# Kernel tuning notes

Hardware: AMD Instinct MI355X
Metric: run time of the kernel (lower is better)

Reference implementation:

```python
import jax, jax.numpy as jnp
import numpy as np

NEG = -1e30


def _layernorm(x, g, b, eps=1e-6):
    mu = jnp.mean(x, axis=-1, keepdims=True)
    var = jnp.mean((x - mu) ** 2, axis=-1, keepdims=True)
    return (x - mu) * jax.lax.rsqrt(var + eps) * g + b


def _ctc_loss(log_probs, targets, input_lengths, target_lengths, blank):
    # log_probs: (T, B, V); targets: (B, L) int; lengths: (B,) int
    T, B, V = log_probs.shape
    L = targets.shape[1]
    S = 2 * L + 1
    # extended target sequence: blank, t0, blank, t1, ..., blank
    ext = jnp.full((B, S), blank, dtype=targets.dtype)
    ext = ext.at[:, 1::2].set(targets)
    # skip transition allowed where label differs from label two back and is not blank
    ext_m2 = jnp.pad(ext, ((0, 0), (2, 0)), constant_values=blank)[:, :S]
    skip_mask = (jnp.arange(S)[None, :] >= 2) & (ext != ext_m2) & (ext != blank)
    # gather per-step emission log-probs for extended labels: (T, B, S)
    lp_ext = jnp.take_along_axis(
        log_probs, jnp.broadcast_to(ext[None], (T, B, S)), axis=2
    )

    alpha0 = jnp.full((B, S), NEG, dtype=log_probs.dtype)
    alpha0 = alpha0.at[:, 0].set(lp_ext[0, :, 0])
    alpha0 = alpha0.at[:, 1].set(lp_ext[0, :, 1])

    def step(alpha, lp_e):
        a1 = jnp.pad(alpha, ((0, 0), (1, 0)), constant_values=NEG)[:, :S]
        a2 = jnp.pad(alpha, ((0, 0), (2, 0)), constant_values=NEG)[:, :S]
        a2 = jnp.where(skip_mask, a2, NEG)
        new = jnp.logaddexp(jnp.logaddexp(alpha, a1), a2) + lp_e
        return new, new

    _, alphas_rest = jax.lax.scan(step, alpha0, lp_ext[1:])
    alphas = jnp.concatenate([alpha0[None], alphas_rest], axis=0)  # (T, B, S)

    alpha_T = alphas[input_lengths - 1, jnp.arange(B)]  # (B, S)
    s_end = 2 * target_lengths  # final blank position
    l_blank = jnp.take_along_axis(alpha_T, s_end[:, None], axis=1)[:, 0]
    l_label = jnp.take_along_axis(alpha_T, (s_end - 1)[:, None], axis=1)[:, 0]
    loss_b = -jnp.logaddexp(l_blank, l_label)
    # zero_infinity=True
    loss_b = jnp.where(loss_b > 1e29, 0.0, loss_b)
    # reduction='mean': divide each loss by its target length, then batch-mean
    return jnp.mean(loss_b / target_lengths.astype(loss_b.dtype))


def setup_inputs() -> dict:
    T, B, D, V, L = 2000, 32, 768, 1024, 150
    key = jax.random.key(0)
    ks = jax.random.split(key, 8)
    s = 0.02
    return {
        "source_encoder_output": jax.random.normal(ks[0], (T, B, D), jnp.float32),
        "W_proj": jax.random.normal(ks[1], (D, D), jnp.float32) * s,
        "b_proj": jnp.zeros((D,), jnp.float32),
        "W_tr": jax.random.normal(ks[2], (D, D), jnp.float32) * s,
        "b_tr": jnp.zeros((D,), jnp.float32),
        "ln_g": jnp.ones((D,), jnp.float32),
        "ln_b": jnp.zeros((D,), jnp.float32),
        "W_dec": jax.random.normal(ks[3], (D, V), jnp.float32) * s,
        "b_dec": jnp.zeros((V,), jnp.float32),
        "target_syllabe_ids": jax.random.randint(ks[4], (B, L), 1, V, jnp.int32),
        "source_encoder_output_lengths": jnp.full((B,), T, jnp.int32),
        "target_syllabe_id_lengths": jnp.full((B,), L, jnp.int32),
    }


def reference(source_encoder_output, W_proj, b_proj, W_tr, b_tr, ln_g, ln_b,
              W_dec, b_dec, target_syllabe_ids, source_encoder_output_lengths,
              target_syllabe_id_lengths):
    BLANK = 0
    x = source_encoder_output @ W_proj + b_proj          # encoder_projection
    x = jax.nn.gelu(x @ W_tr + b_tr, approximate=False)  # transform dense + gelu
    x = _layernorm(x, ln_g, ln_b, eps=1e-6)
    scores = x @ W_dec + b_dec                           # acoustic_decoder
    log_probs = jax.nn.log_softmax(scores, axis=-1)      # (T, B, V)
    return _ctc_loss(log_probs, target_syllabe_ids,
                     source_encoder_output_lengths,
                     target_syllabe_id_lengths, BLANK)
```

## Files before the change

### kernel.cpp

```cpp
#include <hip/hip_runtime.h>
#include <hip/hip_bf16.h>
#include <math.h>
#include <stdint.h>

#define NEGF (-1e30f)
#define LOG2E 1.44269504088896340736f
#define LN2 0.69314718055994530942f

#define LPROW 512

typedef short bf16x8 __attribute__((ext_vector_type(8)));
typedef float f32x4 __attribute__((ext_vector_type(4)));

__device__ __forceinline__ unsigned short f2b(float x) {
  __hip_bfloat16 h = __float2bfloat16(x);
  return *reinterpret_cast<unsigned short*>(&h);
}
__device__ __forceinline__ float b2f(unsigned short u) {
  __hip_bfloat16 h;
  *reinterpret_cast<unsigned short*>(&h) = u;
  return __bfloat162float(h);
}
__device__ __forceinline__ float gelu_exact(float x) {
  return 0.5f * x * (1.0f + erff(x * 0.70710678118654752440f));
}

#if __has_builtin(__builtin_amdgcn_logf)
__device__ __forceinline__ float fast_log2(float x) { return __builtin_amdgcn_logf(x); }
#else
__device__ __forceinline__ float fast_log2(float x) { return log2f(x); }
#endif

template<int CTRL>
__device__ __forceinline__ float dpp_shr(float x) {
  return __int_as_float(__builtin_amdgcn_update_dpp(
      0, __float_as_int(x), 0x110 | CTRL, 0xf, 0xf, true));
}
__device__ __forceinline__ float readlane_f(float x, int l) {
  return __int_as_float(__builtin_amdgcn_readlane(__float_as_int(x), l));
}

__device__ __forceinline__ uint4 gload_x4(const void* p) {
  uint4 r;
  asm volatile("global_load_dwordx4 %0, %1, off" : "=v"(r) : "v"(p));
  return r;
}

__device__ __forceinline__ void gload16(void* lds, const void* g) {
  __builtin_amdgcn_global_load_lds(
      (__attribute__((address_space(1))) void*)(uintptr_t)g,
      (__attribute__((address_space(3))) void*)(unsigned int)(uintptr_t)lds,
      16, 0, 0);
}

__global__ __launch_bounds__(256) void cvt_enc_kernel(
    const float* __restrict__ in, unsigned short* __restrict__ out, long n4)
{
  long i = (long)blockIdx.x * blockDim.x + threadIdx.x;
  const long stride = (long)gridDim.x * blockDim.x;
  for (; i < n4; i += stride) {
    float4 v = ((const float4*)in)[i];
    ushort4 o;
    o.x = f2b(v.x); o.y = f2b(v.y); o.z = f2b(v.z); o.w = f2b(v.w);
    ((ushort4*)out)[i] = o;
  }
}

__global__ __launch_bounds__(256) void cvt_wt_kernel(
    const float* __restrict__ W, unsigned short* __restrict__ WT, int K, int N)
{
  __shared__ float tile[32][33];
  const int n0 = blockIdx.x * 32, k0 = blockIdx.y * 32;
  const int tx = threadIdx.x, ty = threadIdx.y;
#pragma unroll
  for (int i = 0; i < 32; i += 8) {
    int k = k0 + ty + i, n = n0 + tx;
    tile[ty + i][tx] = (k < K && n < N) ? W[(long)k * N + n] : 0.f;
  }
  __syncthreads();
#pragma unroll
  for (int i = 0; i < 32; i += 8) {
    int n = n0 + ty + i, k = k0 + tx;
    if (n < N && k < K) WT[(long)n * K + k] = f2b(tile[tx][ty + i]);
  }
}

template<int NFULL, int EPI>
__global__ __launch_bounds__(256, 2) void gemm128_kernel(
    const unsigned short* __restrict__ A,
    const unsigned short* __restrict__ WT,
    const float* __restrict__ bias,
    unsigned short* __restrict__ out,
    float2* __restrict__ partials,
    int K)
{
  extern __shared__ char smem[];
  unsigned short* As = (unsigned short*)smem;
  unsigned short* Bs = (unsigned short*)(smem + 16384);

  const int tid = threadIdx.x, lane = tid & 63, w = tid >> 6;
  const int wr = w >> 1, wc = w & 1;
  const int cl = lane & 15, g = lane >> 4;
  const int bx = blockIdx.x;
  const long row0 = (long)blockIdx.y * 128;
  const int col0 = bx * 128;

  const int ch0 = w * 64 + lane;
  const int ch1 = 256 + ch0;
  const unsigned short* Ag0 = A + (row0 + (ch0 >> 2)) * K + (ch0 & 3) * 8;
  const unsigned short* Ag1 = A + (row0 + (ch1 >> 2)) * K + (ch1 & 3) * 8;
  const unsigned short* Bg0 = WT + (long)(col0 + (ch0 >> 2)) * K + (ch0 & 3) * 8;
  const unsigned short* Bg1 = WT + (long)(col0 + (ch1 >> 2)) * K + (ch1 & 3) * 8;
  unsigned short* Al0 = As + w * 512;
  unsigned short* Al1 = As + 2048 + w * 512;
  unsigned short* Bl0 = Bs + w * 512;
  unsigned short* Bl1 = Bs + 2048 + w * 512;

#define STAGE(buf, kt)                          \
  do {                                          \
    const int _ko = (kt) * 32;                  \
    gload16(Al0 + (buf) * 4096, Ag0 + _ko);     \
    gload16(Al1 + (buf) * 4096, Ag1 + _ko);     \
    gload16(Bl0 + (buf) * 4096, Bg0 + _ko);     \
    gload16(Bl1 + (buf) * 4096, Bg1 + _ko);     \
  } while (0)

  f32x4 acc[4][4];
#pragma unroll
  for (int mt = 0; mt < 4; ++mt)
#pragma unroll
    for (int nt = 0; nt < 4; ++nt) acc[mt][nt] = (f32x4){0.f, 0.f, 0.f, 0.f};

  const int NKT = K / 32;
  STAGE(0, 0);
  __syncthreads();
  int buf = 0;
  for (int kt = 0; kt < NKT; ++kt) {
    if (kt + 1 < NKT) STAGE(buf ^ 1, kt + 1);
    const unsigned short* Ab = As + buf * 4096;
    const unsigned short* Bb = Bs + buf * 4096;
    bf16x8 af[4], bfr[4];
#pragma unroll
    for (int mt = 0; mt < 4; ++mt)
      af[mt] = *(const bf16x8*)&Ab[(((wr * 64 + mt * 16 + cl) << 2) + g) * 8];
#pragma unroll
    for (int nt = 0; nt < 4; ++nt)
      bfr[nt] = *(const bf16x8*)&Bb[(((wc * 64 + nt * 16 + cl) << 2) + g) * 8];
#pragma unroll
    for (int mt = 0; mt < 4; ++mt)
#pragma unroll
      for (int nt = 0; nt < 4; ++nt)
        acc[mt][nt] = __builtin_amdgcn_mfma_f32_16x16x32_bf16(
            af[mt], bfr[nt], acc[mt][nt], 0, 0, 0);
    __syncthreads();
    buf ^= 1;
  }
#undef STAGE

  float bv[4];
#pragma unroll
  for (int nt = 0; nt < 4; ++nt) bv[nt] = bias[col0 + wc * 64 + nt * 16 + cl];
#pragma unroll
  for (int mt = 0; mt < 4; ++mt)
#pragma unroll
    for (int nt = 0; nt < 4; ++nt)
#pragma unroll
      for (int j = 0; j < 4; ++j) {
        float v = acc[mt][nt][j] + bv[nt];
        if (EPI == 1) v = gelu_exact(v);
        acc[mt][nt][j] = v;
      }

  if (EPI == 2) {
#pragma unroll
    for (int mt = 0; mt < 4; ++mt)
#pragma unroll
      for (int j = 0; j < 4; ++j) {
        float mx = fmaxf(fmaxf(acc[mt][0][j], acc[mt][1][j]),
                         fmaxf(acc[mt][2][j], acc[mt][3][j]));
#pragma unroll
        for (int off = 1; off < 16; off <<= 1)
          mx = fmaxf(mx, __shfl_xor(mx, off));
        float sm = 0.f;
#pragma unroll
        for (int nt = 0; nt < 4; ++nt) sm += expf(acc[mt][nt][j] - mx);
#pragma unroll
        for (int off = 1; off < 16; off <<= 1) sm += __shfl_xor(sm, off);
        if (cl == 0) {
          long m = row0 + wr * 64 + mt * 16 + g * 4 + j;
          partials[m * 16 + bx * 2 + wc] = make_float2(mx, sm);
        }
      }
  }

  unsigned short* Ct = (unsigned short*)smem;
#pragma unroll
  for (int mt = 0; mt < 4; ++mt)
#pragma unroll
    for (int nt = 0; nt < 4; ++nt)
#pragma unroll
      for (int j = 0; j < 4; ++j)
        Ct[(wr * 64 + mt * 16 + g * 4 + j) * 136 + wc * 64 + nt * 16 + cl] =
            f2b(acc[mt][nt][j]);
  __syncthreads();
  for (int idx = tid; idx < 2048; idx += 256) {
    int r = idx >> 4, ch = idx & 15;
    *(bf16x8*)&out[(row0 + r) * NFULL + col0 + ch * 8] =
        *(const bf16x8*)&Ct[r * 136 + ch * 8];
  }
}

template<int D>
__global__ __launch_bounds__(256) void ln_bf16_kernel(
    unsigned short* __restrict__ X, const float* __restrict__ g,
    const float* __restrict__ bt, long M)
{
  constexpr int NI = D / 256;
  const int lane = threadIdx.x & 63;
  const int wid = threadIdx.x >> 6;
  const long row = (long)blockIdx.x * 4 + wid;
  if (row >= M) return;

  float v[NI * 4];
  float s = 0.f;
#pragma unroll
  for (int i = 0; i < NI; ++i) {
    ushort4 u = *(const ushort4*)&X[row * D + (i * 64 + lane) * 4];
    v[i * 4 + 0] = b2f(u.x); v[i * 4 + 1] = b2f(u.y);
    v[i * 4 + 2] = b2f(u.z); v[i * 4 + 3] = b2f(u.w);
    s += v[i * 4 + 0] + v[i * 4 + 1] + v[i * 4 + 2] + v[i * 4 + 3];
  }
#pragma unroll
  for (int off = 32; off; off >>= 1) s += __shfl_xor(s, off);
  const float mu = s * (1.0f / D);
  float q = 0.f;
#pragma unroll
  for (int i = 0; i < NI * 4; ++i) { float d = v[i] - mu; q += d * d; }
#pragma unroll
  for (int off = 32; off; off >>= 1) q += __shfl_xor(q, off);
  const float rs = rsqrtf(q * (1.0f / D) + 1e-6f);
#pragma unroll
  for (int i = 0; i < NI; ++i) {
    ushort4 o;
    int c = (i * 64 + lane) * 4;
    o.x = f2b((v[i * 4 + 0] - mu) * rs * g[c + 0] + bt[c + 0]);
    o.y = f2b((v[i * 4 + 1] - mu) * rs * g[c + 1] + bt[c + 1]);
    o.z = f2b((v[i * 4 + 2] - mu) * rs * g[c + 2] + bt[c + 2]);
    o.w = f2b((v[i * 4 + 3] - mu) * rs * g[c + 3] + bt[c + 3]);
    *(ushort4*)&X[row * D + c] = o;
  }
}

__global__ __launch_bounds__(256) void logz_gather_kernel(
    const unsigned short* __restrict__ scores,
    const float2* __restrict__ partials,
    const int* __restrict__ targets,
    unsigned short* __restrict__ lp_ext,
    long Mtot, int T, int B, int L, int S)
{
  const int w = threadIdx.x >> 6, lane = threadIdx.x & 63;
  const long m = (long)blockIdx.x * 4 + w;
  if (m >= Mtot) return;

  float2 pp = partials[m * 16 + (lane & 15)];
  float Mx = pp.x, Sv = pp.y;
#pragma unroll
  for (int off = 1; off < 16; off <<= 1) {
    float Mo = __shfl_xor(Mx, off);
    float So = __shfl_xor(Sv, off);
    float Mn = fmaxf(Mx, Mo);
    Sv = Sv * expf(Mx - Mn) + So * expf(Mo - Mn);
    Mx = Mn;
  }
  const float logz = Mx + logf(Sv);
  const int b = (int)(m % B);
  const int t = (int)(m / B);
  const unsigned short* srow = scores + m * 1024;
  bf16x8 o = {0, 0, 0, 0, 0, 0, 0, 0};
#pragma unroll
  for (int j = 0; j < 5; ++j) {
    int s = lane * 5 + j;
    if (s < S) {
      int lab = (s & 1) ? targets[b * L + (s >> 1)] : 0;
      o[j] = (short)f2b(expf(b2f(srow[lab]) - logz) * 1024.0f);
    }
  }
  *(bf16x8*)&lp_ext[((long)b * T + t) * LPROW + lane * 8] = o;
}

#define CTC_DEPTH 16
__global__ __launch_bounds__(64, 1) void ctc_scan_kernel(
    const unsigned short* __restrict__ pr,
    const int* __restrict__ targets, const int* __restrict__ inlens,
    const int* __restrict__ tlens, float* __restrict__ partial,
    int T, int B, int L, int S)
{
  const int b = blockIdx.x;
  const int lane = threadIdx.x;
  const int s0 = lane * 5;
  const int inlen = inlens[b];
  const int tlen = tlens[b];
  const int send = 2 * tlen;
  const int capT = inlen - 1;
  const bool is16 = (lane == 16), is32 = (lane == 32), is48 = (lane == 48);

  const unsigned short* lpb = pr + (long)b * T * LPROW + lane * 8;

  float skm[5];
#pragma unroll
  for (int j = 0; j < 5; ++j) {
    int s = s0 + j;
    float sk = 0.f;
    if (s < S && (s & 1) && s >= 3) {
      int lab = targets[b * L + (s >> 1)];
      int lab2 = targets[b * L + (s >> 1) - 1];
      sk = ((lab != 0) && (lab != lab2)) ? 1.f : 0.f;
    }
    skm[j] = sk;
  }

  float a[5];
  float abv = 0.f, alv = 0.f;
  int corr = 0, corr_cap = 0;
#pragma unroll
  for (int j = 0; j < 5; ++j) {
    int s = s0 + j;
    a[j] = (s <= 1) ? b2f(lpb[j]) : 0.f;
  }
  if (capT == 0) {
#pragma unroll
    for (int j = 0; j < 5; ++j) {
      int s = s0 + j;
      if (s == send) abv = a[j];
      if (s == send - 1) alv = a[j];
    }
    corr_cap = corr;
  }

#define CTC_PROCESS(rd, tcur)                                                 \
  do {                                                                        \
    float p0 = __uint_as_float((rd).x << 16);                                 \
    float p1 = __uint_as_float((rd).x & 0xffff0000u);                         \
    float p2 = __uint_as_float((rd).y << 16);                                 \
    float p3 = __uint_as_float((rd).y & 0xffff0000u);                         \
    float p4 = __uint_as_float((rd).z << 16);                                 \
    float r15 = readlane_f(a[4], 15), r31 = readlane_f(a[4], 31),             \
          r47 = readlane_f(a[4], 47);                                         \
    float q15 = readlane_f(a[3], 15), q31 = readlane_f(a[3], 31),             \
          q47 = readlane_f(a[3], 47);                                         \
    float o_m1 = dpp_shr<1>(a[4]);                                            \
    float o_m2 = dpp_shr<1>(a[3]);                                            \
    o_m1 = is16 ? r15 : o_m1; o_m1 = is32 ? r31 : o_m1;                       \
    o_m1 = is48 ? r47 : o_m1;                                                 \
    o_m2 = is16 ? q15 : o_m2; o_m2 = is32 ? q31 : o_m2;                       \
    o_m2 = is48 ? q47 : o_m2;                                                 \
    float na0 = fmaf(skm[0], o_m2, a[0] + o_m1) * p0;                         \
    float na1 = fmaf(skm[1], o_m1, a[1] + a[0]) * p1;                         \
    float na2 = fmaf(skm[2], a[0], a[2] + a[1]) * p2;                         \
    float na3 = fmaf(skm[3], a[1], a[3] + a[2]) * p3;                         \
    float na4 = fmaf(skm[4], a[2], a[4] + a[3]) * p4;                         \
    a[0] = na0; a[1] = na1; a[2] = na2; a[3] = na3; a[4] = na4;               \
    if ((tcur) == capT) {                                                     \
      _Pragma("unroll")                                                       \
      for (int j = 0; j < 5; ++j) {                                           \
        int s = s0 + j;                                                       \
        if (s == send) abv = a[j];                                            \
        if (s == send - 1) alv = a[j];                                        \
      }                                                                       \
      corr_cap = corr;                                                        \
    }                                                                         \
  } while (0)

#define CTC_RENORM                                                            \
  do {                                                                        \
    float m_ = fmaxf(fmaxf(fmaxf(a[0], a[1]), fmaxf(a[2], a[3])), a[4]);      \
    m_ = fmaxf(m_, dpp_shr<1>(m_));                                           \
    m_ = fmaxf(m_, dpp_shr<2>(m_));                                           \
    m_ = fmaxf(m_, dpp_shr<4>(m_));                                           \
    m_ = fmaxf(m_, dpp_shr<8>(m_));                                           \
    float mx = fmaxf(fmaxf(readlane_f(m_, 15), readlane_f(m_, 31)),           \
                     fmaxf(readlane_f(m_, 47), readlane_f(m_, 63)));          \
    int e;                                                                    \
    (void)frexpf(mx, &e);                      \
    float sc = ldexpf(1.f, -e);                                               \
    _Pragma("unroll")                                                         \
    for (int j = 0; j < 5; ++j) a[j] *= sc;                                   \
    corr += e;                                                                \
  } while (0)

  uint4 ring[CTC_DEPTH];
#pragma unroll
  for (int d = 0; d < CTC_DEPTH; ++d)
    ring[d] = gload_x4(lpb + (long)(1 + d) * LPROW);

  const int NCH = (T - 1 + CTC_DEPTH - 1) / CTC_DEPTH;
  int t = 1;
  for (int c = 0; c < NCH; ++c) {
#pragma unroll
    for (int d = 0; d < CTC_DEPTH; ++d) {
      asm volatile("s_waitcnt vmcnt(15)" ::: "memory");
      __builtin_amdgcn_sched_barrier(0);
      if (t < T) CTC_PROCESS(ring[d], t);
      ring[d] = gload_x4(lpb + (long)(t + CTC_DEPTH) * LPROW);
      if ((d & 7) == 7) CTC_RENORM;
      ++t;
    }
  }
  asm volatile("s_waitcnt vmcnt(0)" ::: "memory");

#pragma unroll
  for (int off = 32; off; off >>= 1) {
    abv = fmaxf(abv, __shfl_xor(abv, off));
    alv = fmaxf(alv, __shfl_xor(alv, off));
  }
  if (lane == 0) {
    float l2 = fast_log2(abv + alv) + (float)corr_cap - 10.0f * (float)inlen;
    float loss = -LN2 * l2;
    if (!(loss <= 1e29f)) loss = 0.f;
    partial[b] = loss / (float)tlen;
  }
}

__global__ void reduce_kernel(const float* __restrict__ partial,
                              float* __restrict__ out, int B)
{
  int lane = threadIdx.x;
  float v = (lane < B) ? partial[lane] : 0.f;
#pragma unroll
  for (int off = 32; off; off >>= 1) v += __shfl_xor(v, off);
  if (lane == 0) out[0] = v / (float)B;
}

extern "C" void kernel_launch(void* const* d_in, const int* in_sizes, int n_in,
                              void* d_out, int out_size, void* d_ws, size_t ws_size,
                              hipStream_t stream) {
  const float* enc = (const float*)d_in[0];
  const float* Wp  = (const float*)d_in[1];
  const float* bp  = (const float*)d_in[2];
  const float* Wt  = (const float*)d_in[3];
  const float* btr = (const float*)d_in[4];
  const float* lng = (const float*)d_in[5];
  const float* lnb = (const float*)d_in[6];
  const float* Wd  = (const float*)d_in[7];
  const float* bd  = (const float*)d_in[8];
  const int* tgt   = (const int*)d_in[9];
  const int* inl   = (const int*)d_in[10];
  const int* tll   = (const int*)d_in[11];

  const int D = in_sizes[2];
  const int V = in_sizes[8];
  const int B = in_sizes[10];
  const int L = in_sizes[9] / B;
  const long M = (long)in_sizes[0] / D;
  const int T = (int)(M / B);
  const int S = 2 * L + 1;

  char* wsb = (char*)d_ws;
  size_t off = 0;
  auto alloc = [&](size_t bytes) { char* p = wsb + off; off += (bytes + 255) & ~(size_t)255; return p; };
  unsigned short* encb   = (unsigned short*)alloc((size_t)M * D * 2);
  char* x1region         = alloc((size_t)M * V * 2);
  unsigned short* X1b    = (unsigned short*)x1region;
  unsigned short* scores = (unsigned short*)x1region;
  unsigned short* X2b    = encb;
  unsigned short* LP     = (unsigned short*)alloc((size_t)B * T * LPROW * 2 + 65536);
  float2* partials       = (float2*)alloc((size_t)M * 16 * sizeof(float2));
  unsigned short* WpT    = (unsigned short*)alloc((size_t)D * D * 2);
  unsigned short* WtT    = (unsigned short*)alloc((size_t)D * D * 2);
  unsigned short* WdT    = (unsigned short*)alloc((size_t)D * V * 2);
  float* partial         = (float*)alloc(256);

  cvt_wt_kernel<<<dim3(D / 32, D / 32), dim3(32, 8), 0, stream>>>(Wp, WpT, D, D);
  cvt_wt_kernel<<<dim3(D / 32, D / 32), dim3(32, 8), 0, stream>>>(Wt, WtT, D, D);
  cvt_wt_kernel<<<dim3(V / 32, D / 32), dim3(32, 8), 0, stream>>>(Wd, WdT, D, V);
  cvt_enc_kernel<<<2048, 256, 0, stream>>>(enc, encb, (long)M * D / 4);

  const size_t smemg = 34816;
  const dim3 g12(D / 128, (unsigned)(M / 128));
  const dim3 g3(V / 128, (unsigned)(M / 128));

  gemm128_kernel<768, 0><<<g12, 256, smemg, stream>>>(encb, WpT, bp, X1b, nullptr, D);
  gemm128_kernel<768, 1><<<g12, 256, smemg, stream>>>(X1b, WtT, btr, X2b, nullptr, D);
  ln_bf16_kernel<768><<<(int)(M / 4), 256, 0, stream>>>(X2b, lng, lnb, M);
  gemm128_kernel<1024, 2><<<g3, 256, smemg, stream>>>(X2b, WdT, bd, scores, partials, D);

  logz_gather_kernel<<<(int)(M / 4), 256, 0, stream>>>(
      scores, partials, tgt, LP, M, T, B, L, S);
  ctc_scan_kernel<<<B, 64, 0, stream>>>(LP, tgt, inl, tll, partial, T, B, L, S);
  reduce_kernel<<<1, 64, 0, stream>>>(partial, (float*)d_out, B);
}
```

Measured before the change: 806.9 us.

## Remap GEMM workgroups XCD-aware and shrink CTC prefetch ring to eight named registers

```diff
diff --git a/kernel.cpp b/kernel.cpp
--- a/kernel.cpp
+++ b/kernel.cpp
@@ -92,7 +92,7 @@
     const float* __restrict__ bias,
     unsigned short* __restrict__ out,
     float2* __restrict__ partials,
-    int K)
+    int K, int gx, int nwg)
 {
   extern __shared__ char smem[];
   unsigned short* As = (unsigned short*)smem;
@@ -101,8 +101,10 @@
   const int tid = threadIdx.x, lane = tid & 63, w = tid >> 6;
   const int wr = w >> 1, wc = w & 1;
   const int cl = lane & 15, g = lane >> 4;
-  const int bx = blockIdx.x;
-  const long row0 = (long)blockIdx.y * 128;
+  const int bid = blockIdx.x;
+  const int wid = (bid & 7) * (nwg >> 3) + (bid >> 3);
+  const int bx = wid % gx;
+  const long row0 = (long)(wid / gx) * 128;
   const int col0 = bx * 128;
 
   const int ch0 = w * 64 + lane;
@@ -288,7 +290,6 @@
   *(bf16x8*)&lp_ext[((long)b * T + t) * LPROW + lane * 8] = o;
 }
 
-#define CTC_DEPTH 16
 __global__ __launch_bounds__(64, 1) void ctc_scan_kernel(
     const unsigned short* __restrict__ pr,
     const int* __restrict__ targets, const int* __restrict__ inlens,
@@ -336,6 +337,12 @@
     }
     corr_cap = corr;
   }
+
+#define CTC_WAIT                                          \
+  do {                                                    \
+    asm volatile("s_waitcnt vmcnt(7)" ::: "memory");      \
+    __builtin_amdgcn_sched_barrier(0);                    \
+  } while (0)
 
 #define CTC_PROCESS(rd, tcur)                                                 \
   do {                                                                        \
@@ -388,23 +395,35 @@
     corr += e;                                                                \
   } while (0)
 
-  uint4 ring[CTC_DEPTH];
-#pragma unroll
-  for (int d = 0; d < CTC_DEPTH; ++d)
-    ring[d] = gload_x4(lpb + (long)(1 + d) * LPROW);
-
-  const int NCH = (T - 1 + CTC_DEPTH - 1) / CTC_DEPTH;
+#define CTC_STEP(gN)                                          \
+  do {                                                        \
+    CTC_WAIT;                                                 \
+    if (t < T) CTC_PROCESS(gN, t);                            \
+    gN = gload_x4(lpb + (long)(t + 8) * LPROW);               \
+    ++t;                                                      \
+  } while (0)
+
+  uint4 g0 = gload_x4(lpb + (long)1 * LPROW);
+  uint4 g1 = gload_x4(lpb + (long)2 * LPROW);
+  uint4 g2 = gload_x4(lpb + (long)3 * LPROW);
+  uint4 g3 = gload_x4(lpb + (long)4 * LPROW);
+  uint4 g4 = gload_x4(lpb + (long)5 * LPROW);
+  uint4 g5 = gload_x4(lpb + (long)6 * LPROW);
+  uint4 g6 = gload_x4(lpb + (long)7 * LPROW);
+  uint4 g7 = gload_x4(lpb + (long)8 * LPROW);
+
+  const int NCH = (T - 1 + 7) / 8;
   int t = 1;
   for (int c = 0; c < NCH; ++c) {
-#pragma unroll
-    for (int d = 0; d < CTC_DEPTH; ++d) {
-      asm volatile("s_waitcnt vmcnt(15)" ::: "memory");
-      __builtin_amdgcn_sched_barrier(0);
-      if (t < T) CTC_PROCESS(ring[d], t);
-      ring[d] = gload_x4(lpb + (long)(t + CTC_DEPTH) * LPROW);
-      if ((d & 7) == 7) CTC_RENORM;
-      ++t;
-    }
+    CTC_STEP(g0);
+    CTC_STEP(g1);
+    CTC_STEP(g2);
+    CTC_STEP(g3);
+    CTC_STEP(g4);
+    CTC_STEP(g5);
+    CTC_STEP(g6);
+    CTC_STEP(g7);
+    CTC_RENORM;
   }
   asm volatile("s_waitcnt vmcnt(0)" ::: "memory");
 
@@ -476,13 +495,16 @@
   cvt_enc_kernel<<<2048, 256, 0, stream>>>(enc, encb, (long)M * D / 4);
 
   const size_t smemg = 34816;
-  const dim3 g12(D / 128, (unsigned)(M / 128));
-  const dim3 g3(V / 128, (unsigned)(M / 128));
-
-  gemm128_kernel<768, 0><<<g12, 256, smemg, stream>>>(encb, WpT, bp, X1b, nullptr, D);
-  gemm128_kernel<768, 1><<<g12, 256, smemg, stream>>>(X1b, WtT, btr, X2b, nullptr, D);
+  const int gx12 = D / 128, nwg12 = gx12 * (int)(M / 128);
+  const int gx3 = V / 128, nwg3 = gx3 * (int)(M / 128);
+
+  gemm128_kernel<768, 0><<<nwg12, 256, smemg, stream>>>(
+      encb, WpT, bp, X1b, nullptr, D, gx12, nwg12);
+  gemm128_kernel<768, 1><<<nwg12, 256, smemg, stream>>>(
+      X1b, WtT, btr, X2b, nullptr, D, gx12, nwg12);
   ln_bf16_kernel<768><<<(int)(M / 4), 256, 0, stream>>>(X2b, lng, lnb, M);
-  gemm128_kernel<1024, 2><<<g3, 256, smemg, stream>>>(X2b, WdT, bd, scores, partials, D);
+  gemm128_kernel<1024, 2><<<nwg3, 256, smemg, stream>>>(
+      X2b, WdT, bd, scores, partials, D, gx3, nwg3);
 
   logz_gather_kernel<<<(int)(M / 4), 256, 0, stream>>>(
       scores, partials, tgt, LP, M, T, B, L, S);
```

New measurement: 772.9 us. 4.2% less time.
